# Performance work log

Measured on AMD Instinct MI355X. Metric: run time of the kernel, lower is better.

The kernel has to match this reference:

```python
import jax, jax.numpy as jnp
import numpy as np

N_NODES = 20000
N_EDGES = 320000
IN_FEATS = 128
HID = 32
HEADS1 = 8
OUT_FEATS = 64


def _segment_softmax(logits, seg, num_segments):
    # logits: [E, H] grouped by destination node `seg`
    m = jax.ops.segment_max(logits, seg, num_segments=num_segments)  # [N, H]
    e = jnp.exp(logits - m[seg])
    s = jax.ops.segment_sum(e, seg, num_segments=num_segments)  # [N, H]
    return e / (s[seg] + 1e-16)


def _gat_conv(x, edge_index, W, a_src, a_dst, b, heads, ch, concat, neg_slope):
    # x: [N, F_in]; W: [F_in, heads*ch]; a_src/a_dst: [heads, ch]; b: [heads*ch] or [ch]
    N = x.shape[0]
    # add self-loops (PyG GATConv default add_self_loops=True)
    loop = jnp.arange(N, dtype=edge_index.dtype)
    src = jnp.concatenate([edge_index[0], loop])
    dst = jnp.concatenate([edge_index[1], loop])

    h = (x @ W).reshape(N, heads, ch)                      # [N, H, C]
    alpha_src = jnp.einsum('nhc,hc->nh', h, a_src)          # [N, H]
    alpha_dst = jnp.einsum('nhc,hc->nh', h, a_dst)          # [N, H]

    alpha = jax.nn.leaky_relu(alpha_src[src] + alpha_dst[dst], neg_slope)  # [E', H]
    alpha = _segment_softmax(alpha, dst, N)                 # [E', H]

    msg = h[src] * alpha[:, :, None]                        # [E', H, C]
    out = jax.ops.segment_sum(msg, dst, num_segments=N)     # [N, H, C]

    if concat:
        out = out.reshape(N, heads * ch)
    else:
        out = out.mean(axis=1)
    return out + b


def setup_inputs() -> dict:
    key = jax.random.key(0)
    ks = jax.random.split(key, 10)
    x = jax.random.normal(ks[0], (N_NODES, IN_FEATS), dtype=jnp.float32)
    edge_index = jax.random.randint(ks[1], (2, N_EDGES), 0, N_NODES, dtype=jnp.int32)

    def glorot(k, shape):
        fan = sum(shape[-2:]) if len(shape) > 1 else shape[-1]
        return jax.random.normal(k, shape, dtype=jnp.float32) * jnp.sqrt(2.0 / fan)

    W1 = glorot(ks[2], (IN_FEATS, HEADS1 * HID))
    a_src1 = glorot(ks[3], (HEADS1, HID))
    a_dst1 = glorot(ks[4], (HEADS1, HID))
    b1 = jnp.zeros((HEADS1 * HID,), dtype=jnp.float32)
    W2 = glorot(ks[5], (HEADS1 * HID, OUT_FEATS))
    a_src2 = glorot(ks[6], (1, OUT_FEATS))
    a_dst2 = glorot(ks[7], (1, OUT_FEATS))
    b2 = jnp.zeros((OUT_FEATS,), dtype=jnp.float32)
    return {"x": x, "W1": W1, "a_src1": a_src1, "a_dst1": a_dst1, "b1": b1,
            "W2": W2, "a_src2": a_src2, "a_dst2": a_dst2, "b2": b2,
            "edge_index": edge_index}


def reference(x, W1, a_src1, a_dst1, b1, W2, a_src2, a_dst2, b2, edge_index):
    h = _gat_conv(x, edge_index, W1, a_src1, a_dst1, b1,
                  heads=HEADS1, ch=HID, concat=True, neg_slope=0.2)
    h = jax.nn.leaky_relu(h, 0.01)  # F.leaky_relu default slope
    out = _gat_conv(h, edge_index, W2, a_src2, a_dst2, b2,
                    heads=1, ch=OUT_FEATS, concat=False, neg_slope=0.2)
    return out
```

## Files before the change

### kernel.cpp

```cpp
#include <hip/hip_runtime.h>
#include <hip/hip_fp16.h>

#define NN 20000
#define NE 320000
#define EP (NE + NN)
#define FIN 128
#define HEADS 8
#define HID 32
#define C1 256
#define C2 64
#define CAP 128

typedef _Float16 f16;
typedef __attribute__((ext_vector_type(8))) _Float16 f16x8;
typedef __attribute__((ext_vector_type(4))) _Float16 f16x4;
typedef __attribute__((ext_vector_type(4))) float f32x4;

__global__ void k_prep(const float* __restrict__ x, f16* __restrict__ x16,
                       const float* __restrict__ W1, const float* __restrict__ W2,
                       f16* __restrict__ W1T, f16* __restrict__ W2T,
                       int* __restrict__ cnt) {
    int i = blockIdx.x * 256 + threadIdx.x;
    const int NX = NN * FIN / 4;
    if (i < NX) {
        float4 v = ((const float4*)x)[i];
        f16x4 h = {(_Float16)v.x, (_Float16)v.y, (_Float16)v.z, (_Float16)v.w};
        ((f16x4*)x16)[i] = h;
        return;
    }
    int j = i - NX;
    if (j < FIN * C1) {
        int k = j >> 8, n = j & 255;
        W1T[n * FIN + k] = (f16)W1[j];
        return;
    }
    j -= FIN * C1;
    if (j < C1 * C2) {
        int k = j >> 6, n = j & 63;
        W2T[n * C1 + k] = (f16)W2[j];
        return;
    }
    j -= C1 * C2;
    if (j < NN) cnt[j] = 0;
}

__global__ void k_bucket(const int* __restrict__ ei, int* __restrict__ cnt,
                         int* __restrict__ bucket) {
    int e = blockIdx.x * 256 + threadIdx.x;
    if (e >= EP) return;
    int src, dst;
    if (e < NE) { src = ei[e]; dst = ei[NE + e]; }
    else { src = dst = e - NE; }
    int pos = atomicAdd(&cnt[dst], 1);
    if (pos < CAP) bucket[(size_t)dst * CAP + pos] = src;
}

__device__ __forceinline__ int swz(int row, int kb) {
    return (row * 64 + kb) ^ ((row & 7) << 4);
}

template <typename OT, int MODE>
__global__ __launch_bounds__(256) void k_mgemm(const f16* __restrict__ A,
                                               const f16* __restrict__ BT,
                                               OT* __restrict__ C, int M, int N, int K,
                                               const float* __restrict__ a_src,
                                               const float* __restrict__ a_dst,
                                               float* __restrict__ as_o,
                                               float* __restrict__ ad_o) {
    __shared__ char lds[8192];
    __shared__ float sred[64][2];
    char* as = lds;
    char* bs = lds + 4096;
    const int t = threadIdx.x;
    const int bm = blockIdx.y * 64;
    const int bn = blockIdx.x * 64;
    const int srow = t >> 2;
    const int skb = (t & 3) * 16;
    const int sk8 = (t & 3) * 8;
    const int l = t & 63;
    const int w = t >> 6;
    const int wr = (w >> 1) * 32, wc = (w & 1) * 32;
    const int lr = l & 15, lg = l >> 4;
    f32x4 acc00 = {}, acc01 = {}, acc10 = {}, acc11 = {};
    const bool arow_ok = (bm + srow) < M;
    const f16* gA = A + (size_t)(bm + srow) * K + sk8;
    const f16* gB = BT + (size_t)(bn + srow) * K + sk8;
    for (int k0 = 0; k0 < K; k0 += 32) {
        f16x8 av = {};
        if (arow_ok) av = *(const f16x8*)(gA + k0);
        f16x8 bv = *(const f16x8*)(gB + k0);
        __syncthreads();
        *(f16x8*)(as + swz(srow, skb)) = av;
        *(f16x8*)(bs + swz(srow, skb)) = bv;
        __syncthreads();
        f16x8 a0 = *(f16x8*)(as + swz(wr + lr, lg * 16));
        f16x8 a1 = *(f16x8*)(as + swz(wr + 16 + lr, lg * 16));
        f16x8 b0 = *(f16x8*)(bs + swz(wc + lr, lg * 16));
        f16x8 b1 = *(f16x8*)(bs + swz(wc + 16 + lr, lg * 16));
        acc00 = __builtin_amdgcn_mfma_f32_16x16x32_f16(a0, b0, acc00, 0, 0, 0);
        acc01 = __builtin_amdgcn_mfma_f32_16x16x32_f16(a0, b1, acc01, 0, 0, 0);
        acc10 = __builtin_amdgcn_mfma_f32_16x16x32_f16(a1, b0, acc10, 0, 0, 0);
        acc11 = __builtin_amdgcn_mfma_f32_16x16x32_f16(a1, b1, acc11, 0, 0, 0);
    }
    const int crow0 = bm + wr + lg * 4;
    const int ccol0 = bn + wc + lr;
#pragma unroll
    for (int r = 0; r < 4; ++r) {
        int r0 = crow0 + r;
        if (r0 < M) {
            C[(size_t)r0 * N + ccol0] = (OT)acc00[r];
            C[(size_t)r0 * N + ccol0 + 16] = (OT)acc01[r];
        }
        int r1 = r0 + 16;
        if (r1 < M) {
            C[(size_t)r1 * N + ccol0] = (OT)acc10[r];
            C[(size_t)r1 * N + ccol0 + 16] = (OT)acc11[r];
        }
    }
    if constexpr (MODE == 1) {
        const float av0 = a_src[ccol0], av1 = a_src[ccol0 + 16];
        const float dv0 = a_dst[ccol0], dv1 = a_dst[ccol0 + 16];
        const int head = (bn + wc) >> 5;
#pragma unroll
        for (int r = 0; r < 4; ++r) {
            float ps0 = acc00[r] * av0 + acc01[r] * av1;
            float pd0 = acc00[r] * dv0 + acc01[r] * dv1;
            float ps1 = acc10[r] * av0 + acc11[r] * av1;
            float pd1 = acc10[r] * dv0 + acc11[r] * dv1;
#pragma unroll
            for (int off = 1; off < 16; off <<= 1) {
                ps0 += __shfl_xor(ps0, off, 16);
                pd0 += __shfl_xor(pd0, off, 16);
                ps1 += __shfl_xor(ps1, off, 16);
                pd1 += __shfl_xor(pd1, off, 16);
            }
            if (lr == 0) {
                int row0 = crow0 + r, row1 = row0 + 16;
                if (row0 < M) { as_o[row0 * HEADS + head] = ps0; ad_o[row0 * HEADS + head] = pd0; }
                if (row1 < M) { as_o[row1 * HEADS + head] = ps1; ad_o[row1 * HEADS + head] = pd1; }
            }
        }
    }
    if constexpr (MODE == 2) {
        const float av0 = a_src[ccol0], av1 = a_src[ccol0 + 16];
        const float dv0 = a_dst[ccol0], dv1 = a_dst[ccol0 + 16];
        float psl[8], pdl[8];
#pragma unroll
        for (int r = 0; r < 4; ++r) {
            psl[r]     = acc00[r] * av0 + acc01[r] * av1;
            pdl[r]     = acc00[r] * dv0 + acc01[r] * dv1;
            psl[r + 4] = acc10[r] * av0 + acc11[r] * av1;
            pdl[r + 4] = acc10[r] * dv0 + acc11[r] * dv1;
        }
#pragma unroll
        for (int i = 0; i < 8; ++i) {
#pragma unroll
            for (int off = 1; off < 16; off <<= 1) {
                psl[i] += __shfl_xor(psl[i], off, 16);
                pdl[i] += __shfl_xor(pdl[i], off, 16);
            }
        }
        if (((w & 1) == 0) && lr == 0) {
#pragma unroll
            for (int r = 0; r < 4; ++r) {
                int row0 = wr + lg * 4 + r, row1 = row0 + 16;
                sred[row0][0] = psl[r];     sred[row0][1] = pdl[r];
                sred[row1][0] = psl[r + 4]; sred[row1][1] = pdl[r + 4];
            }
        }
        __syncthreads();
        if (((w & 1) == 1) && lr == 0) {
#pragma unroll
            for (int r = 0; r < 4; ++r) {
                int row0 = wr + lg * 4 + r, row1 = row0 + 16;
                int g0 = bm + row0, g1 = bm + row1;
                if (g0 < M) { as_o[g0] = sred[row0][0] + psl[r];     ad_o[g0] = sred[row0][1] + pdl[r]; }
                if (g1 < M) { as_o[g1] = sred[row1][0] + psl[r + 4]; ad_o[g1] = sred[row1][1] + pdl[r + 4]; }
            }
        }
    }
}

__global__ void k_agg1(const f16* __restrict__ h1h, const float* __restrict__ as1,
                       const float* __restrict__ ad1, const int* __restrict__ cnt,
                       const int* __restrict__ bucket, const float* __restrict__ b1,
                       f16* __restrict__ out) {
    const int t = threadIdx.x & 63;
    const int n = (blockIdx.x << 2) + (threadIdx.x >> 6);
    const int h = t >> 3;
    int deg = cnt[n];
    deg = (deg < CAP) ? deg : CAP;
    const int* __restrict__ row = bucket + (size_t)n * CAP;
    const float adn = ad1[n * HEADS + h];
    float s = 0.f;
    float a0 = 0.f, a1 = 0.f, a2 = 0.f, a3 = 0.f;
    int j = 0;
    for (; j + 4 <= deg; j += 4) {
        const int s0 = row[j], s1 = row[j + 1];
        const int s2 = row[j + 2], s3 = row[j + 3];
        float x0 = as1[s0 * HEADS + h] + adn;
        float x1 = as1[s1 * HEADS + h] + adn;
        float x2 = as1[s2 * HEADS + h] + adn;
        float x3 = as1[s3 * HEADS + h] + adn;
        f16x4 q0 = ((const f16x4*)(h1h + (size_t)s0 * C1))[t];
        f16x4 q1 = ((const f16x4*)(h1h + (size_t)s1 * C1))[t];
        f16x4 q2 = ((const f16x4*)(h1h + (size_t)s2 * C1))[t];
        f16x4 q3 = ((const f16x4*)(h1h + (size_t)s3 * C1))[t];
        x0 = (x0 > 0.f) ? x0 : 0.2f * x0;
        x1 = (x1 > 0.f) ? x1 : 0.2f * x1;
        x2 = (x2 > 0.f) ? x2 : 0.2f * x2;
        x3 = (x3 > 0.f) ? x3 : 0.2f * x3;
        const float w0 = expf(x0), w1 = expf(x1), w2 = expf(x2), w3 = expf(x3);
        s += (w0 + w1) + (w2 + w3);
        a0 += (float)q0[0] * w0 + (float)q1[0] * w1 + (float)q2[0] * w2 + (float)q3[0] * w3;
        a1 += (float)q0[1] * w0 + (float)q1[1] * w1 + (float)q2[1] * w2 + (float)q3[1] * w3;
        a2 += (float)q0[2] * w0 + (float)q1[2] * w1 + (float)q2[2] * w2 + (float)q3[2] * w3;
        a3 += (float)q0[3] * w0 + (float)q1[3] * w1 + (float)q2[3] * w2 + (float)q3[3] * w3;
    }
    for (; j < deg; ++j) {
        const int s0 = row[j];
        float x = as1[s0 * HEADS + h] + adn;
        x = (x > 0.f) ? x : 0.2f * x;
        const float w = expf(x);
        f16x4 q = ((const f16x4*)(h1h + (size_t)s0 * C1))[t];
        s += w;
        a0 += (float)q[0] * w; a1 += (float)q[1] * w;
        a2 += (float)q[2] * w; a3 += (float)q[3] * w;
    }
    const float inv = 1.f / (s + 1e-16f);
    const float4 bv = ((const float4*)b1)[t];
    float o0 = a0 * inv + bv.x, o1 = a1 * inv + bv.y;
    float o2 = a2 * inv + bv.z, o3 = a3 * inv + bv.w;
    o0 = (o0 > 0.f) ? o0 : 0.01f * o0;
    o1 = (o1 > 0.f) ? o1 : 0.01f * o1;
    o2 = (o2 > 0.f) ? o2 : 0.01f * o2;
    o3 = (o3 > 0.f) ? o3 : 0.01f * o3;
    f16x4 o16 = {(_Float16)o0, (_Float16)o1, (_Float16)o2, (_Float16)o3};
    ((f16x4*)(out + (size_t)n * C1))[t] = o16;
}

__global__ void k_agg2(const f16* __restrict__ h2h, const float* __restrict__ as2,
                       const float* __restrict__ ad2, const int* __restrict__ cnt,
                       const int* __restrict__ bucket, const float* __restrict__ b2,
                       float* __restrict__ out) {
    const int t = threadIdx.x & 63;
    const int n = (blockIdx.x << 2) + (threadIdx.x >> 6);
    int deg = cnt[n];
    deg = (deg < CAP) ? deg : CAP;
    const int* __restrict__ row = bucket + (size_t)n * CAP;
    const float adn = ad2[n];
    float s = 0.f, acc = 0.f;
    int j = 0;
    for (; j + 4 <= deg; j += 4) {
        const int s0 = row[j], s1 = row[j + 1];
        const int s2 = row[j + 2], s3 = row[j + 3];
        float x0 = as2[s0] + adn, x1 = as2[s1] + adn;
        float x2 = as2[s2] + adn, x3 = as2[s3] + adn;
        const float g0 = (float)h2h[(size_t)s0 * C2 + t];
        const float g1 = (float)h2h[(size_t)s1 * C2 + t];
        const float g2 = (float)h2h[(size_t)s2 * C2 + t];
        const float g3 = (float)h2h[(size_t)s3 * C2 + t];
        x0 = (x0 > 0.f) ? x0 : 0.2f * x0;
        x1 = (x1 > 0.f) ? x1 : 0.2f * x1;
        x2 = (x2 > 0.f) ? x2 : 0.2f * x2;
        x3 = (x3 > 0.f) ? x3 : 0.2f * x3;
        const float w0 = expf(x0), w1 = expf(x1), w2 = expf(x2), w3 = expf(x3);
        s += (w0 + w1) + (w2 + w3);
        acc += g0 * w0 + g1 * w1 + g2 * w2 + g3 * w3;
    }
    for (; j < deg; ++j) {
        const int s0 = row[j];
        float x = as2[s0] + adn;
        x = (x > 0.f) ? x : 0.2f * x;
        const float w = expf(x);
        s += w;
        acc += (float)h2h[(size_t)s0 * C2 + t] * w;
    }
    out[(size_t)n * C2 + t] = acc * (1.f / (s + 1e-16f)) + b2[t];
}

extern "C" void kernel_launch(void* const* d_in, const int* in_sizes, int n_in,
                              void* d_out, int out_size, void* d_ws, size_t ws_size,
                              hipStream_t stream) {
    const float* x      = (const float*)d_in[0];
    const float* W1     = (const float*)d_in[1];
    const float* a_src1 = (const float*)d_in[2];
    const float* a_dst1 = (const float*)d_in[3];
    const float* b1     = (const float*)d_in[4];
    const float* W2     = (const float*)d_in[5];
    const float* a_src2 = (const float*)d_in[6];
    const float* a_dst2 = (const float*)d_in[7];
    const float* b2     = (const float*)d_in[8];
    const int*   ei     = (const int*)d_in[9];
    float* out = (float*)d_out;

    char* ws = (char*)d_ws;
    size_t off = 0;
    auto alloc = [&](size_t bytes) {
        void* p = ws + off;
        off += (bytes + 255) & ~(size_t)255;
        return p;
    };
    f16*  x16    = (f16*)alloc((size_t)NN * FIN * 2);
    f16*  W1T    = (f16*)alloc((size_t)C1 * FIN * 2);
    f16*  W2T    = (f16*)alloc((size_t)C2 * C1 * 2);
    f16*  h1h    = (f16*)alloc((size_t)NN * C1 * 2);
    f16*  hl2h   = (f16*)alloc((size_t)NN * C1 * 2);
    f16*  h2h    = (f16*)alloc((size_t)NN * C2 * 2);
    float* as1   = (float*)alloc((size_t)NN * HEADS * 4);
    float* ad1   = (float*)alloc((size_t)NN * HEADS * 4);
    float* as2   = (float*)alloc((size_t)NN * 4);
    float* ad2   = (float*)alloc((size_t)NN * 4);
    int*   cnt   = (int*)alloc((size_t)NN * 4);
    int*   bucket= (int*)alloc((size_t)NN * CAP * 4);

    const int EB = (EP + 255) / 256;
    const int PREP_N = NN * FIN / 4 + FIN * C1 + C1 * C2 + NN;

    k_prep<<<(PREP_N + 255) / 256, 256, 0, stream>>>(x, x16, W1, W2, W1T, W2T, cnt);

    k_bucket<<<EB, 256, 0, stream>>>(ei, cnt, bucket);

    k_mgemm<f16, 1><<<dim3(C1 / 64, (NN + 63) / 64), 256, 0, stream>>>(
        x16, W1T, h1h, NN, C1, FIN, a_src1, a_dst1, as1, ad1);
    k_agg1<<<NN / 4, 256, 0, stream>>>(h1h, as1, ad1, cnt, bucket, b1, hl2h);

    k_mgemm<f16, 2><<<dim3(C2 / 64, (NN + 63) / 64), 256, 0, stream>>>(
        hl2h, W2T, h2h, NN, C2, C1, a_src2, a_dst2, as2, ad2);
    k_agg2<<<NN / 4, 256, 0, stream>>>(h2h, as2, ad2, cnt, bucket, b2, out);
}
```

Measured before the change: 96.88 us.

## Merge prep and bucketing kernels; use fewer lanes per node in aggregations

Combines the conversion/transposition kernel with the edge-bucketing kernel into one launch and zeroes the degree counters with a memset first. In layer-1 aggregation each node now gets 32 lanes loading 8 halves each, instead of 64 lanes loading 4. In layer-2 aggregation each node gets 16 lanes loading 4 halves and writing float4, instead of 64 lanes doing scalar loads. The goal is fewer launches, wider gathers and more nodes per block, at the cost of more registers per thread.

```diff
diff --git a/kernel.cpp b/kernel.cpp
--- a/kernel.cpp
+++ b/kernel.cpp
@@ -16,37 +16,39 @@
 typedef __attribute__((ext_vector_type(4))) _Float16 f16x4;
 typedef __attribute__((ext_vector_type(4))) float f32x4;
 
-__global__ void k_prep(const float* __restrict__ x, f16* __restrict__ x16,
-                       const float* __restrict__ W1, const float* __restrict__ W2,
-                       f16* __restrict__ W1T, f16* __restrict__ W2T,
-                       int* __restrict__ cnt) {
-    int i = blockIdx.x * 256 + threadIdx.x;
-    const int NX = NN * FIN / 4;
-    if (i < NX) {
-        float4 v = ((const float4*)x)[i];
-        f16x4 h = {(_Float16)v.x, (_Float16)v.y, (_Float16)v.z, (_Float16)v.w};
-        ((f16x4*)x16)[i] = h;
+#define NX (NN * FIN / 4)
+#define PREP_T (NX + FIN * C1 + C1 * C2)
+#define PREP_BLKS ((PREP_T + 255) / 256)
+#define EB ((EP + 255) / 256)
+
+__global__ void k_prepbucket(const float* __restrict__ x, f16* __restrict__ x16,
+                             const float* __restrict__ W1, const float* __restrict__ W2,
+                             f16* __restrict__ W1T, f16* __restrict__ W2T,
+                             const int* __restrict__ ei, int* __restrict__ cnt,
+                             int* __restrict__ bucket) {
+    const int b = blockIdx.x;
+    if (b < PREP_BLKS) {
+        int i = b * 256 + threadIdx.x;
+        if (i < NX) {
+            float4 v = ((const float4*)x)[i];
+            f16x4 h = {(_Float16)v.x, (_Float16)v.y, (_Float16)v.z, (_Float16)v.w};
+            ((f16x4*)x16)[i] = h;
+            return;
+        }
+        int j = i - NX;
+        if (j < FIN * C1) {
+            int k = j >> 8, n = j & 255;
+            W1T[n * FIN + k] = (f16)W1[j];
+            return;
+        }
+        j -= FIN * C1;
+        if (j < C1 * C2) {
+            int k = j >> 6, n = j & 63;
+            W2T[n * C1 + k] = (f16)W2[j];
+        }
         return;
     }
-    int j = i - NX;
-    if (j < FIN * C1) {
-        int k = j >> 8, n = j & 255;
-        W1T[n * FIN + k] = (f16)W1[j];
-        return;
-    }
-    j -= FIN * C1;
-    if (j < C1 * C2) {
-        int k = j >> 6, n = j & 63;
-        W2T[n * C1 + k] = (f16)W2[j];
-        return;
-    }
-    j -= C1 * C2;
-    if (j < NN) cnt[j] = 0;
-}
-
-__global__ void k_bucket(const int* __restrict__ ei, int* __restrict__ cnt,
-                         int* __restrict__ bucket) {
-    int e = blockIdx.x * 256 + threadIdx.x;
+    int e = (b - PREP_BLKS) * 256 + threadIdx.x;
     if (e >= EP) return;
     int src, dst;
     if (e < NE) { src = ei[e]; dst = ei[NE + e]; }
@@ -185,27 +187,84 @@
                        const float* __restrict__ ad1, const int* __restrict__ cnt,
                        const int* __restrict__ bucket, const float* __restrict__ b1,
                        f16* __restrict__ out) {
-    const int t = threadIdx.x & 63;
-    const int n = (blockIdx.x << 2) + (threadIdx.x >> 6);
-    const int h = t >> 3;
+    const int l = threadIdx.x & 31;
+    const int n = (blockIdx.x << 3) + (threadIdx.x >> 5);
+    const int h = l >> 2;
     int deg = cnt[n];
     deg = (deg < CAP) ? deg : CAP;
     const int* __restrict__ row = bucket + (size_t)n * CAP;
     const float adn = ad1[n * HEADS + h];
     float s = 0.f;
+    float a[8] = {};
+    int j = 0;
+    for (; j + 4 <= deg; j += 4) {
+        const int i0 = row[j], i1 = row[j + 1], i2 = row[j + 2], i3 = row[j + 3];
+        float x0 = as1[i0 * HEADS + h] + adn;
+        float x1 = as1[i1 * HEADS + h] + adn;
+        float x2 = as1[i2 * HEADS + h] + adn;
+        float x3 = as1[i3 * HEADS + h] + adn;
+        f16x8 q0 = ((const f16x8*)(h1h + (size_t)i0 * C1))[l];
+        f16x8 q1 = ((const f16x8*)(h1h + (size_t)i1 * C1))[l];
+        f16x8 q2 = ((const f16x8*)(h1h + (size_t)i2 * C1))[l];
+        f16x8 q3 = ((const f16x8*)(h1h + (size_t)i3 * C1))[l];
+        x0 = (x0 > 0.f) ? x0 : 0.2f * x0;
+        x1 = (x1 > 0.f) ? x1 : 0.2f * x1;
+        x2 = (x2 > 0.f) ? x2 : 0.2f * x2;
+        x3 = (x3 > 0.f) ? x3 : 0.2f * x3;
+        const float w0 = expf(x0), w1 = expf(x1), w2 = expf(x2), w3 = expf(x3);
+        s += (w0 + w1) + (w2 + w3);
+#pragma unroll
+        for (int c = 0; c < 8; ++c)
+            a[c] += (float)q0[c] * w0 + (float)q1[c] * w1 + (float)q2[c] * w2 + (float)q3[c] * w3;
+    }
+    for (; j < deg; ++j) {
+        const int i0 = row[j];
+        float xx = as1[i0 * HEADS + h] + adn;
+        xx = (xx > 0.f) ? xx : 0.2f * xx;
+        const float w = expf(xx);
+        f16x8 q = ((const f16x8*)(h1h + (size_t)i0 * C1))[l];
+        s += w;
+#pragma unroll
+        for (int c = 0; c < 8; ++c) a[c] += (float)q[c] * w;
+    }
+    const float inv = 1.f / (s + 1e-16f);
+    const float4 bv0 = ((const float4*)b1)[2 * l];
+    const float4 bv1 = ((const float4*)b1)[2 * l + 1];
+    float o[8];
+    o[0] = a[0] * inv + bv0.x; o[1] = a[1] * inv + bv0.y;
+    o[2] = a[2] * inv + bv0.z; o[3] = a[3] * inv + bv0.w;
+    o[4] = a[4] * inv + bv1.x; o[5] = a[5] * inv + bv1.y;
+    o[6] = a[6] * inv + bv1.z; o[7] = a[7] * inv + bv1.w;
+    f16x8 o16;
+#pragma unroll
+    for (int c = 0; c < 8; ++c) {
+        float v = (o[c] > 0.f) ? o[c] : 0.01f * o[c];
+        o16[c] = (_Float16)v;
+    }
+    ((f16x8*)(out + (size_t)n * C1))[l] = o16;
+}
+
+__global__ void k_agg2(const f16* __restrict__ h2h, const float* __restrict__ as2,
+                       const float* __restrict__ ad2, const int* __restrict__ cnt,
+                       const int* __restrict__ bucket, const float* __restrict__ b2,
+                       float* __restrict__ out) {
+    const int g = threadIdx.x & 15;
+    const int n = (blockIdx.x << 4) + (threadIdx.x >> 4);
+    int deg = cnt[n];
+    deg = (deg < CAP) ? deg : CAP;
+    const int* __restrict__ row = bucket + (size_t)n * CAP;
+    const float adn = ad2[n];
+    float s = 0.f;
     float a0 = 0.f, a1 = 0.f, a2 = 0.f, a3 = 0.f;
     int j = 0;
     for (; j + 4 <= deg; j += 4) {
-        const int s0 = row[j], s1 = row[j + 1];
-        const int s2 = row[j + 2], s3 = row[j + 3];
-        float x0 = as1[s0 * HEADS + h] + adn;
-        float x1 = as1[s1 * HEADS + h] + adn;
-        float x2 = as1[s2 * HEADS + h] + adn;
-        float x3 = as1[s3 * HEADS + h] + adn;
-        f16x4 q0 = ((const f16x4*)(h1h + (size_t)s0 * C1))[t];
-        f16x4 q1 = ((const f16x4*)(h1h + (size_t)s1 * C1))[t];
-        f16x4 q2 = ((const f16x4*)(h1h + (size_t)s2 * C1))[t];
-        f16x4 q3 = ((const f16x4*)(h1h + (size_t)s3 * C1))[t];
+        const int i0 = row[j], i1 = row[j + 1], i2 = row[j + 2], i3 = row[j + 3];
+        float x0 = as2[i0] + adn, x1 = as2[i1] + adn;
+        float x2 = as2[i2] + adn, x3 = as2[i3] + adn;
+        f16x4 q0 = ((const f16x4*)(h2h + (size_t)i0 * C2))[g];
+        f16x4 q1 = ((const f16x4*)(h2h + (size_t)i1 * C2))[g];
+        f16x4 q2 = ((const f16x4*)(h2h + (size_t)i2 * C2))[g];
+        f16x4 q3 = ((const f16x4*)(h2h + (size_t)i3 * C2))[g];
         x0 = (x0 > 0.f) ? x0 : 0.2f * x0;
         x1 = (x1 > 0.f) ? x1 : 0.2f * x1;
         x2 = (x2 > 0.f) ? x2 : 0.2f * x2;
@@ -218,65 +277,23 @@
         a3 += (float)q0[3] * w0 + (float)q1[3] * w1 + (float)q2[3] * w2 + (float)q3[3] * w3;
     }
     for (; j < deg; ++j) {
-        const int s0 = row[j];
-        float x = as1[s0 * HEADS + h] + adn;
-        x = (x > 0.f) ? x : 0.2f * x;
-        const float w = expf(x);
-        f16x4 q = ((const f16x4*)(h1h + (size_t)s0 * C1))[t];
+        const int i0 = row[j];
+        float xx = as2[i0] + adn;
+        xx = (xx > 0.f) ? xx : 0.2f * xx;
+        const float w = expf(xx);
+        f16x4 q = ((const f16x4*)(h2h + (size_t)i0 * C2))[g];
         s += w;
         a0 += (float)q[0] * w; a1 += (float)q[1] * w;
         a2 += (float)q[2] * w; a3 += (float)q[3] * w;
     }
     const float inv = 1.f / (s + 1e-16f);
-    const float4 bv = ((const float4*)b1)[t];
-    float o0 = a0 * inv + bv.x, o1 = a1 * inv + bv.y;
-    float o2 = a2 * inv + bv.z, o3 = a3 * inv + bv.w;
-    o0 = (o0 > 0.f) ? o0 : 0.01f * o0;
-    o1 = (o1 > 0.f) ? o1 : 0.01f * o1;
-    o2 = (o2 > 0.f) ? o2 : 0.01f * o2;
-    o3 = (o3 > 0.f) ? o3 : 0.01f * o3;
-    f16x4 o16 = {(_Float16)o0, (_Float16)o1, (_Float16)o2, (_Float16)o3};
-    ((f16x4*)(out + (size_t)n * C1))[t] = o16;
-}
-
-__global__ void k_agg2(const f16* __restrict__ h2h, const float* __restrict__ as2,
-                       const float* __restrict__ ad2, const int* __restrict__ cnt,
-                       const int* __restrict__ bucket, const float* __restrict__ b2,
-                       float* __restrict__ out) {
-    const int t = threadIdx.x & 63;
-    const int n = (blockIdx.x << 2) + (threadIdx.x >> 6);
-    int deg = cnt[n];
-    deg = (deg < CAP) ? deg : CAP;
-    const int* __restrict__ row = bucket + (size_t)n * CAP;
-    const float adn = ad2[n];
-    float s = 0.f, acc = 0.f;
-    int j = 0;
-    for (; j + 4 <= deg; j += 4) {
-        const int s0 = row[j], s1 = row[j + 1];
-        const int s2 = row[j + 2], s3 = row[j + 3];
-        float x0 = as2[s0] + adn, x1 = as2[s1] + adn;
-        float x2 = as2[s2] + adn, x3 = as2[s3] + adn;
-        const float g0 = (float)h2h[(size_t)s0 * C2 + t];
-        const float g1 = (float)h2h[(size_t)s1 * C2 + t];
-        const float g2 = (float)h2h[(size_t)s2 * C2 + t];
-        const float g3 = (float)h2h[(size_t)s3 * C2 + t];
-        x0 = (x0 > 0.f) ? x0 : 0.2f * x0;
-        x1 = (x1 > 0.f) ? x1 : 0.2f * x1;
-        x2 = (x2 > 0.f) ? x2 : 0.2f * x2;
-        x3 = (x3 > 0.f) ? x3 : 0.2f * x3;
-        const float w0 = expf(x0), w1 = expf(x1), w2 = expf(x2), w3 = expf(x3);
-        s += (w0 + w1) + (w2 + w3);
-        acc += g0 * w0 + g1 * w1 + g2 * w2 + g3 * w3;
-    }
-    for (; j < deg; ++j) {
-        const int s0 = row[j];
-        float x = as2[s0] + adn;
-        x = (x > 0.f) ? x : 0.2f * x;
-        const float w = expf(x);
-        s += w;
-        acc += (float)h2h[(size_t)s0 * C2 + t] * w;
-    }
-    out[(size_t)n * C2 + t] = acc * (1.f / (s + 1e-16f)) + b2[t];
+    const float4 bv = ((const float4*)b2)[g];
+    float4 o;
+    o.x = a0 * inv + bv.x;
+    o.y = a1 * inv + bv.y;
+    o.z = a2 * inv + bv.z;
+    o.w = a3 * inv + bv.w;
+    ((float4*)(out + (size_t)n * C2))[g] = o;
 }
 
 extern "C" void kernel_launch(void* const* d_in, const int* in_sizes, int n_in,
@@ -314,18 +331,16 @@
     int*   cnt   = (int*)alloc((size_t)NN * 4);
     int*   bucket= (int*)alloc((size_t)NN * CAP * 4);
 
-    const int EB = (EP + 255) / 256;
-    const int PREP_N = NN * FIN / 4 + FIN * C1 + C1 * C2 + NN;
-
-    k_prep<<<(PREP_N + 255) / 256, 256, 0, stream>>>(x, x16, W1, W2, W1T, W2T, cnt);
-
-    k_bucket<<<EB, 256, 0, stream>>>(ei, cnt, bucket);
+    hipMemsetAsync(cnt, 0, (size_t)NN * 4, stream);
+
+    k_prepbucket<<<PREP_BLKS + EB, 256, 0, stream>>>(x, x16, W1, W2, W1T, W2T,
+                                                     ei, cnt, bucket);
 
     k_mgemm<f16, 1><<<dim3(C1 / 64, (NN + 63) / 64), 256, 0, stream>>>(
         x16, W1T, h1h, NN, C1, FIN, a_src1, a_dst1, as1, ad1);
-    k_agg1<<<NN / 4, 256, 0, stream>>>(h1h, as1, ad1, cnt, bucket, b1, hl2h);
+    k_agg1<<<NN / 8, 256, 0, stream>>>(h1h, as1, ad1, cnt, bucket, b1, hl2h);
 
     k_mgemm<f16, 2><<<dim3(C2 / 64, (NN + 63) / 64), 256, 0, stream>>>(
         hl2h, W2T, h2h, NN, C2, C1, a_src2, a_dst2, as2, ad2);
-    k_agg2<<<NN / 4, 256, 0, stream>>>(h2h, as2, ad2, cnt, bucket, b2, out);
-}
+    k_agg2<<<NN / 16, 256, 0, stream>>>(h2h, as2, ad2, cnt, bucket, b2, out);
+}
```

New measurement: 91.86 us. 5.2% less time.
